# Performance work log

Hardware: AMD Instinct MI355X
Metric: run time of the kernel (lower is better)

Reference implementation:

```python
import jax, jax.numpy as jnp
import numpy as np


def _haar2d(x):
    # x: (B, C, H, W) -> four subbands (B, C, H//2, W//2)
    B, C, H, W = x.shape
    xb = x.reshape(B, C, H // 2, 2, W // 2, 2)
    a = xb[:, :, :, 0, :, 0]  # top-left
    b = xb[:, :, :, 0, :, 1]  # top-right
    c = xb[:, :, :, 1, :, 0]  # bottom-left
    d = xb[:, :, :, 1, :, 1]  # bottom-right
    LL = (a + b + c + d) * 0.5
    LH = (a - b + c - d) * 0.5
    HL = (a + b - c - d) * 0.5
    HH = (a - b - c + d) * 0.5
    return LL, LH, HL, HH


def setup_inputs() -> dict:
    key = jax.random.key(0)
    k1, k2 = jax.random.split(key)
    shape = (4, 32, 512, 512)
    return {
        "input": jax.random.normal(k1, shape, dtype=jnp.float32),
        "target": jax.random.normal(k2, shape, dtype=jnp.float32),
    }


def reference(input, target):
    in_bands = _haar2d(input)
    tg_bands = _haar2d(target)
    # nn.MSELoss default: mean over all elements, per subband, then summed
    loss = jnp.float32(0.0)
    for ib, tb in zip(in_bands, tg_bands):
        d = ib - tb
        loss = loss + jnp.mean(d * d)
    return loss
```

## Files before the change

### kernel.cpp

```cpp
#include <hip/hip_runtime.h>


typedef float fvec4 __attribute__((ext_vector_type(4)));

#define S1_BLOCK 256
#define S1_ITERS 8
#define S1_CHUNK (S1_BLOCK * S1_ITERS)

__global__ __launch_bounds__(S1_BLOCK) void haar_mse_stage1(
    const fvec4* __restrict__ x,
    const fvec4* __restrict__ t,
    float* __restrict__ ws,
    int n4)
{
    const int tid  = threadIdx.x;
    const int base = blockIdx.x * S1_CHUNK + tid;

    float acc0 = 0.0f, acc1 = 0.0f, acc2 = 0.0f, acc3 = 0.0f;

    if (base + (S1_ITERS - 1) * S1_BLOCK < n4) {
        fvec4 a[S1_ITERS], b[S1_ITERS];
        #pragma unroll
        for (int k = 0; k < S1_ITERS; ++k) {
            a[k] = __builtin_nontemporal_load(&x[base + k * S1_BLOCK]);
            b[k] = __builtin_nontemporal_load(&t[base + k * S1_BLOCK]);
        }
        __builtin_amdgcn_sched_barrier(0);

        #pragma unroll
        for (int k = 0; k < S1_ITERS; ++k) {
            fvec4 d = a[k] - b[k];
            acc0 = fmaf(d.x, d.x, acc0);
            acc1 = fmaf(d.y, d.y, acc1);
            acc2 = fmaf(d.z, d.z, acc2);
            acc3 = fmaf(d.w, d.w, acc3);
        }
    } else {
        for (int k = 0; k < S1_ITERS; ++k) {
            const int i = base + k * S1_BLOCK;
            if (i < n4) {
                fvec4 a = x[i];
                fvec4 b = t[i];
                fvec4 d = a - b;
                acc0 = fmaf(d.x, d.x, acc0);
                acc1 = fmaf(d.y, d.y, acc1);
                acc2 = fmaf(d.z, d.z, acc2);
                acc3 = fmaf(d.w, d.w, acc3);
            }
        }
    }

    float acc = (acc0 + acc1) + (acc2 + acc3);

    #pragma unroll
    for (int off = 32; off > 0; off >>= 1)
        acc += __shfl_down(acc, off, 64);

    __shared__ float wave_sums[4];
    const int wave = tid >> 6;
    const int lane = tid & 63;
    if (lane == 0) wave_sums[wave] = acc;
    __syncthreads();

    if (tid == 0)
        ws[blockIdx.x] = (wave_sums[0] + wave_sums[1]) + (wave_sums[2] + wave_sums[3]);
}

__global__ __launch_bounds__(256) void haar_mse_stage2(
    const float* __restrict__ ws,
    float* __restrict__ out,
    int nblocks,
    float scale)
{
    float s = 0.0f;
    for (int i = threadIdx.x; i < nblocks; i += 256)
        s += ws[i];

    #pragma unroll
    for (int off = 32; off > 0; off >>= 1)
        s += __shfl_down(s, off, 64);

    __shared__ float wave_sums[4];
    const int wave = threadIdx.x >> 6;
    const int lane = threadIdx.x & 63;
    if (lane == 0) wave_sums[wave] = s;
    __syncthreads();

    if (threadIdx.x == 0)
        out[0] = ((wave_sums[0] + wave_sums[1]) + (wave_sums[2] + wave_sums[3])) * scale;
}

extern "C" void kernel_launch(void* const* d_in, const int* in_sizes, int n_in,
                              void* d_out, int out_size, void* d_ws, size_t ws_size,
                              hipStream_t stream) {
    const float* x = (const float*)d_in[0];
    const float* t = (const float*)d_in[1];
    float* out = (float*)d_out;
    float* ws  = (float*)d_ws;

    const int n  = in_sizes[0];
    const int n4 = n / 4;
    const int nblocks = (n4 + S1_CHUNK - 1) / S1_CHUNK;

    haar_mse_stage1<<<nblocks, S1_BLOCK, 0, stream>>>(
        (const fvec4*)x, (const fvec4*)t, ws, n4);

    const float scale = 1.0f / (float)(n / 4);
    haar_mse_stage2<<<1, 256, 0, stream>>>(ws, out, nblocks, scale);
}
```

Measured before the change: 252.7 us.

## Double-buffer stage1 loads in batches and enlarge per-block chunk

```diff
diff --git a/kernel.cpp b/kernel.cpp
--- a/kernel.cpp
+++ b/kernel.cpp
@@ -3,9 +3,10 @@
 
 typedef float fvec4 __attribute__((ext_vector_type(4)));
 
-#define S1_BLOCK 256
-#define S1_ITERS 8
-#define S1_CHUNK (S1_BLOCK * S1_ITERS)
+#define S1_BLOCK   256
+#define S1_DEPTH   4
+#define S1_BATCHES 8
+#define S1_CHUNK   (S1_BLOCK * S1_DEPTH * S1_BATCHES)
 
 __global__ __launch_bounds__(S1_BLOCK) void haar_mse_stage1(
     const fvec4* __restrict__ x,
@@ -18,34 +19,50 @@
 
     float acc0 = 0.0f, acc1 = 0.0f, acc2 = 0.0f, acc3 = 0.0f;
 
-    if (base + (S1_ITERS - 1) * S1_BLOCK < n4) {
-        fvec4 a[S1_ITERS], b[S1_ITERS];
-        #pragma unroll
-        for (int k = 0; k < S1_ITERS; ++k) {
-            a[k] = __builtin_nontemporal_load(&x[base + k * S1_BLOCK]);
-            b[k] = __builtin_nontemporal_load(&t[base + k * S1_BLOCK]);
-        }
-        __builtin_amdgcn_sched_barrier(0);
+    if (blockIdx.x * S1_CHUNK + S1_CHUNK <= n4) {
+        fvec4 a[2][S1_DEPTH], b[2][S1_DEPTH];
 
         #pragma unroll
-        for (int k = 0; k < S1_ITERS; ++k) {
-            fvec4 d = a[k] - b[k];
-            acc0 = fmaf(d.x, d.x, acc0);
-            acc1 = fmaf(d.y, d.y, acc1);
-            acc2 = fmaf(d.z, d.z, acc2);
-            acc3 = fmaf(d.w, d.w, acc3);
+        for (int k = 0; k < S1_DEPTH; ++k) {
+            a[0][k] = __builtin_nontemporal_load(&x[base + k * S1_BLOCK]);
+            b[0][k] = __builtin_nontemporal_load(&t[base + k * S1_BLOCK]);
         }
-    } else {
-        for (int k = 0; k < S1_ITERS; ++k) {
-            const int i = base + k * S1_BLOCK;
-            if (i < n4) {
-                fvec4 a = x[i];
-                fvec4 b = t[i];
-                fvec4 d = a - b;
+
+        #pragma unroll
+        for (int j = 0; j < S1_BATCHES; ++j) {
+            const int cur = j & 1;
+            const int nxt = cur ^ 1;
+            if (j + 1 < S1_BATCHES) {
+                const int nb = base + (j + 1) * (S1_DEPTH * S1_BLOCK);
+                #pragma unroll
+                for (int k = 0; k < S1_DEPTH; ++k) {
+                    a[nxt][k] = __builtin_nontemporal_load(&x[nb + k * S1_BLOCK]);
+                    b[nxt][k] = __builtin_nontemporal_load(&t[nb + k * S1_BLOCK]);
+                }
+            }
+            __builtin_amdgcn_sched_barrier(0);
+            #pragma unroll
+            for (int k = 0; k < S1_DEPTH; ++k) {
+                fvec4 d = a[cur][k] - b[cur][k];
                 acc0 = fmaf(d.x, d.x, acc0);
                 acc1 = fmaf(d.y, d.y, acc1);
                 acc2 = fmaf(d.z, d.z, acc2);
                 acc3 = fmaf(d.w, d.w, acc3);
+            }
+        }
+    } else {
+        for (int j = 0; j < S1_BATCHES; ++j) {
+            for (int k = 0; k < S1_DEPTH; ++k) {
+                const int i = base + j * (S1_DEPTH * S1_BLOCK) + k * S1_BLOCK;
+                if (i < n4) {
+                    fvec4 av = x[i];
+                    fvec4 bv = t[i];
+                    fvec4 d = av - bv;
+                    acc0 = fmaf(d.x, d.x, acc0);
+                    acc1 = fmaf(d.y, d.y, acc1);
+                    acc2 = fmaf(d.z, d.z, acc2);
+                    acc3 = fmaf(d.w, d.w, acc3);
+                }
             }
         }
     }
```

After: 248.4 us (median of 2 runs). About the same (-1.7%).

## Stream inputs through LDS with double-buffered direct global-to-LDS loads

Applied to the files above, without the earlier changes.

```diff
diff --git a/kernel.cpp b/kernel.cpp
--- a/kernel.cpp
+++ b/kernel.cpp
@@ -3,50 +3,73 @@
 
 typedef float fvec4 __attribute__((ext_vector_type(4)));
 
-#define S1_BLOCK 256
-#define S1_ITERS 8
-#define S1_CHUNK (S1_BLOCK * S1_ITERS)
+#define S1_BLOCK  256
+#define S1_ROUNDS 16
+#define S1_RCHUNK S1_BLOCK
+#define S1_CHUNK  (S1_RCHUNK * S1_ROUNDS)
 
-__global__ __launch_bounds__(S1_BLOCK) void haar_mse_stage1(
+typedef const __attribute__((address_space(1))) void g_void;
+typedef __attribute__((address_space(3))) void lds_void;
+
+__global__ __launch_bounds__(S1_BLOCK, 8) void haar_mse_stage1(
     const fvec4* __restrict__ x,
     const fvec4* __restrict__ t,
     float* __restrict__ ws,
     int n4)
 {
+    __shared__ fvec4 bx[2][S1_BLOCK];
+    __shared__ fvec4 bt[2][S1_BLOCK];
+
     const int tid  = threadIdx.x;
-    const int base = blockIdx.x * S1_CHUNK + tid;
+    const int wave = tid >> 6;
+    const int lane = tid & 63;
+    const int woff = wave << 6;
+    const int cbase = blockIdx.x * S1_CHUNK;
 
     float acc0 = 0.0f, acc1 = 0.0f, acc2 = 0.0f, acc3 = 0.0f;
 
-    if (base + (S1_ITERS - 1) * S1_BLOCK < n4) {
-        fvec4 a[S1_ITERS], b[S1_ITERS];
-        #pragma unroll
-        for (int k = 0; k < S1_ITERS; ++k) {
-            a[k] = __builtin_nontemporal_load(&x[base + k * S1_BLOCK]);
-            b[k] = __builtin_nontemporal_load(&t[base + k * S1_BLOCK]);
-        }
-        __builtin_amdgcn_sched_barrier(0);
+    if (cbase + S1_CHUNK <= n4) {
+        const fvec4* gx = x + cbase + woff + lane;
+        const fvec4* gt = t + cbase + woff + lane;
+
+        __builtin_amdgcn_global_load_lds((g_void*)gx, (lds_void*)&bx[0][woff], 16, 0, 0);
+        __builtin_amdgcn_global_load_lds((g_void*)gt, (lds_void*)&bt[0][woff], 16, 0, 0);
 
         #pragma unroll
-        for (int k = 0; k < S1_ITERS; ++k) {
-            fvec4 d = a[k] - b[k];
+        for (int r = 0; r < S1_ROUNDS; ++r) {
+            const int cur = r & 1;
+            const int nxt = cur ^ 1;
+            if (r + 1 < S1_ROUNDS) {
+                __builtin_amdgcn_global_load_lds((g_void*)(gx + (r + 1) * S1_RCHUNK),
+                                                 (lds_void*)&bx[nxt][woff], 16, 0, 0);
+                __builtin_amdgcn_global_load_lds((g_void*)(gt + (r + 1) * S1_RCHUNK),
+                                                 (lds_void*)&bt[nxt][woff], 16, 0, 0);
+                asm volatile("s_waitcnt vmcnt(2)" ::: "memory");
+            } else {
+                asm volatile("s_waitcnt vmcnt(0)" ::: "memory");
+            }
+            __builtin_amdgcn_sched_barrier(0);
+
+            fvec4 a = bx[cur][woff + lane];
+            fvec4 b = bt[cur][woff + lane];
+            fvec4 d = a - b;
             acc0 = fmaf(d.x, d.x, acc0);
             acc1 = fmaf(d.y, d.y, acc1);
             acc2 = fmaf(d.z, d.z, acc2);
             acc3 = fmaf(d.w, d.w, acc3);
+
+            __builtin_amdgcn_sched_barrier(0);
         }
     } else {
-        for (int k = 0; k < S1_ITERS; ++k) {
-            const int i = base + k * S1_BLOCK;
-            if (i < n4) {
-                fvec4 a = x[i];
-                fvec4 b = t[i];
-                fvec4 d = a - b;
-                acc0 = fmaf(d.x, d.x, acc0);
-                acc1 = fmaf(d.y, d.y, acc1);
-                acc2 = fmaf(d.z, d.z, acc2);
-                acc3 = fmaf(d.w, d.w, acc3);
-            }
+        const int end = (cbase + S1_CHUNK < n4) ? (cbase + S1_CHUNK) : n4;
+        for (int i = cbase + tid; i < end; i += S1_BLOCK) {
+            fvec4 a = x[i];
+            fvec4 b = t[i];
+            fvec4 d = a - b;
+            acc0 = fmaf(d.x, d.x, acc0);
+            acc1 = fmaf(d.y, d.y, acc1);
+            acc2 = fmaf(d.z, d.z, acc2);
+            acc3 = fmaf(d.w, d.w, acc3);
         }
     }
 
@@ -57,8 +80,6 @@
         acc += __shfl_down(acc, off, 64);
 
     __shared__ float wave_sums[4];
-    const int wave = tid >> 6;
-    const int lane = tid & 63;
     if (lane == 0) wave_sums[wave] = acc;
     __syncthreads();
 
```

Measured after the change: 280.0 us. 1.11x slower.
